# Optimization experiments

Measured on AMD Instinct MI355X. Metric: run time of the kernel, lower is better.

## Reference

```python
import jax, jax.numpy as jnp
import numpy as np

N = 32768      # points (multiple of block_size)
D = 32         # h_dim (dim_per_head, also token feature dim)
H = 8          # num_heads
C = 3          # n_hashes
BS = 128       # block_size
R = 3          # coords_dim
K = 8          # num_w_per_dist
NB = N // BS   # buckets
EPS_LN = 1e-5


def _ln(x, w, b):
    mu = x.mean(-1, keepdims=True)
    var = ((x - mu) ** 2).mean(-1, keepdims=True)
    return (x - mu) * jax.lax.rsqrt(var + EPS_LN) * w + b


def setup_inputs() -> dict:
    key = jax.random.key(0)
    ks = jax.random.split(key, 16)
    s = 0.05
    return {
        "x": jax.random.normal(ks[0], (N, D), jnp.float32),
        "coords": jax.random.uniform(ks[1], (N, R), jnp.float32),
        "combined_shifts": jax.random.randint(ks[2], (C, H, N), 0, 2048),
        "norm1_w": jnp.ones((D,), jnp.float32),
        "norm1_b": jnp.zeros((D,), jnp.float32),
        "wq": s * jax.random.normal(ks[3], (D, H * D), jnp.float32),
        "wk": s * jax.random.normal(ks[4], (D, H * D), jnp.float32),
        "wv": s * jax.random.normal(ks[5], (D, H * D), jnp.float32),
        "w_rpe_w": s * jax.random.normal(ks[6], (H * D, R * K), jnp.float32),
        "alpha": jax.random.normal(ks[7], (H, D + R, C), jnp.float32),  # E2LSH (frozen)
        "out_w": s * jax.random.normal(ks[8], (H * D, D), jnp.float32),
        "out_b": jnp.zeros((D,), jnp.float32),
        "norm2_w": jnp.ones((D,), jnp.float32),
        "norm2_b": jnp.zeros((D,), jnp.float32),
        "ff1_w": s * jax.random.normal(ks[9], (D, D), jnp.float32),
        "ff1_b": jnp.zeros((D,), jnp.float32),
        "ff2_w": s * jax.random.normal(ks[10], (D, D), jnp.float32),
        "ff2_b": jnp.zeros((D,), jnp.float32),
    }


def _to_buckets(v, perm):
    # v: [H, N, d], perm: [C, H, N] -> [C, H, NB, BS, d]
    g = jnp.take_along_axis(v[None], perm[..., None], axis=2)
    return g.reshape(C, H, NB, BS, v.shape[-1])


def _from_buckets(s, inv):
    # s: [C, H, NB, BS, d], inv: [C, H, N] -> [C, H, N, d]
    f = s.reshape(C, H, N, s.shape[-1])
    return jnp.take_along_axis(f, inv[..., None], axis=2)


def _hept_forward(x, coords, combined_shifts, norm1_w, norm1_b, wq, wk, wv,
                  w_rpe_w, alpha, out_w, out_b, norm2_w, norm2_b,
                  ff1_w, ff1_b, ff2_w, ff2_b):
    xn = _ln(x, norm1_w, norm1_b)
    q = (xn @ wq).reshape(N, H, D)
    k = (xn @ wk).reshape(N, H, D)
    v = (xn @ wv).reshape(N, H, D)

    # prep_qk: RPE-derived kernel coordinates
    w = w_rpe_w.reshape(H, D, R, K)                       # (h d) (r k) -> h d r k
    qw = jnp.exp(jnp.minimum(w.sum(axis=1), 50.0)).sum(-1)  # [H, R]
    sqrt_w_r = jnp.sqrt(2.0 * qw)[None] * coords[:, None]    # [N, H, R]
    q_hat = jnp.concatenate([q, sqrt_w_r], axis=-1)          # [N, H, D+R]
    k_hat = jnp.concatenate([k, sqrt_w_r], axis=-1)

    q_hat = jnp.transpose(q_hat, (1, 0, 2))  # [H, N, D+R]
    k_hat = jnp.transpose(k_hat, (1, 0, 2))
    val = jnp.transpose(v, (1, 0, 2))        # [H, N, D]

    # LSH hashing (no-grad in original; outputs only feed integer argsort)
    qh = jax.lax.stop_gradient(jnp.einsum('hnd,hdc->chn', q_hat, alpha))
    kh = jax.lax.stop_gradient(jnp.einsum('hnd,hdc->chn', k_hat, alpha))
    hi = jnp.maximum(qh.max(-1, keepdims=True), kh.max(-1, keepdims=True))
    lo = jnp.minimum(qh.min(-1, keepdims=True), kh.min(-1, keepdims=True))
    hash_shift = hi - lo                                    # [C, H, 1]
    shift = combined_shifts.astype(qh.dtype) * hash_shift
    q_pos = jnp.argsort(qh + shift, axis=-1)                # [C, H, N]
    k_pos = jnp.argsort(kh + shift, axis=-1)

    s_query = _to_buckets(q_hat, q_pos)
    s_key = _to_buckets(k_hat, k_pos)
    s_value = _to_buckets(val, k_pos)

    # kernelized exponential attention within buckets
    q_sq = -0.5 * (s_query ** 2).sum(-1, keepdims=True)
    k_sq = -0.5 * (s_key ** 2).sum(-1, keepdims=True)
    dists = jnp.einsum('chbid,chbjd->chbij', s_query, s_key)
    qk = jnp.exp(jnp.minimum(dists + q_sq + jnp.swapaxes(k_sq, -1, -2), 0.0))
    denom = qk.sum(-1, keepdims=True) + 1e-20
    so = jnp.einsum('chbij,chbjd->chbid', qk, s_value)

    q_rev = jnp.argsort(q_pos, axis=-1)  # inverse permutation
    o = _from_buckets(so, q_rev).sum(0)        # [H, N, D]
    logits = _from_buckets(denom, q_rev).sum(0)  # [H, N, 1]
    out = o / logits

    out = jnp.transpose(out, (1, 0, 2)).reshape(N, H * D) @ out_w + out_b
    x = x + out  # dropout is identity in eval
    xn2 = _ln(x, norm2_w, norm2_b)
    ff = jax.nn.silu(xn2 @ ff1_w + ff1_b) @ ff2_w + ff2_b
    return x + ff


def reference(x, coords, combined_shifts, norm1_w, norm1_b, wq, wk, wv,
              w_rpe_w, alpha, out_w, out_b, norm2_w, norm2_b,
              ff1_w, ff1_b, ff2_w, ff2_b):
    return _hept_forward(x, coords, combined_shifts, norm1_w, norm1_b, wq, wk, wv,
                         w_rpe_w, alpha, out_w, out_b, norm2_w, norm2_b,
                         ff1_w, ff1_b, ff2_w, ff2_b)
```

## Files before the change

kernel.cpp:

```cpp
#include <hip/hip_runtime.h>

#define NPTS 32768
#define DIM 32
#define NH 8
#define NC 3
#define BSZ 128
#define NB 256
#define DH 35
#define DP 36
#define NSEG 24

typedef unsigned long long ull;
typedef __attribute__((ext_vector_type(8))) short bf16x8;
typedef __attribute__((ext_vector_type(4))) float f32x4;

__device__ __forceinline__ unsigned fmap(float f){
  unsigned b = __float_as_uint(f);
  return (b & 0x80000000u) ? ~b : (b | 0x80000000u);
}
__device__ __forceinline__ float funmap(unsigned u){
  unsigned b = (u & 0x80000000u) ? (u & 0x7fffffffu) : ~u;
  return __uint_as_float(b);
}
__device__ __forceinline__ unsigned short f2bf(float f){
  unsigned u = __float_as_uint(f);
  u += 0x7fffu + ((u >> 16) & 1u);
  return (unsigned short)(u >> 16);
}
__device__ __forceinline__ float bf2f(unsigned short h){
  return __uint_as_float(((unsigned)h) << 16);
}
__device__ __forceinline__ void cvt8(const float* f, bf16x8& hi, bf16x8& lo){
  #pragma unroll
  for (int j = 0; j < 8; ++j){
    unsigned short hb = f2bf(f[j]);
    hi[j] = (short)hb;
    lo[j] = (short)f2bf(f[j] - bf2f(hb));
  }
}

__device__ __forceinline__ void cswap(ull& a, ull& b, bool up){
  if ((a > b) == up){ ull t = a; a = b; b = t; }
}
__device__ __forceinline__ void bitonic8_initial(ull r[8], unsigned gbase){
  #pragma unroll
  for (int p = 0; p < 4; ++p){
    bool up = (((gbase + 2*p) & 2) == 0);
    cswap(r[2*p], r[2*p+1], up);
  }
  #pragma unroll
  for (int b = 0; b < 2; ++b){
    bool up = (((gbase + 4*b) & 4) == 0);
    cswap(r[4*b+0], r[4*b+2], up);
    cswap(r[4*b+1], r[4*b+3], up);
    cswap(r[4*b+0], r[4*b+1], up);
    cswap(r[4*b+2], r[4*b+3], up);
  }
  bool up = ((gbase & 8) == 0);
  #pragma unroll
  for (int i = 0; i < 4; ++i) cswap(r[i], r[i+4], up);
  #pragma unroll
  for (int b = 0; b < 2; ++b){
    cswap(r[4*b+0], r[4*b+2], up);
    cswap(r[4*b+1], r[4*b+3], up);
  }
  #pragma unroll
  for (int p = 0; p < 4; ++p) cswap(r[2*p], r[2*p+1], up);
}
__device__ __forceinline__ void bitonic8_finish(ull r[8], bool up){
  #pragma unroll
  for (int i = 0; i < 4; ++i) cswap(r[i], r[i+4], up);
  #pragma unroll
  for (int b = 0; b < 2; ++b){
    cswap(r[4*b+0], r[4*b+2], up);
    cswap(r[4*b+1], r[4*b+3], up);
  }
  #pragma unroll
  for (int p = 0; p < 4; ++p) cswap(r[2*p], r[2*p+1], up);
}

__global__ __launch_bounds__(256) void k_prep(const float* __restrict__ w_rpe,
        float* __restrict__ qw_sqrt, unsigned* __restrict__ slots_hi,
        unsigned* __restrict__ slots_lo){
  int tid = threadIdx.x;
  if (tid < NSEG){ slots_hi[tid] = 0u; slots_lo[tid] = 0xFFFFFFFFu; }
  __shared__ float S[24][8];
  if (tid < 192){
    int hr = tid >> 3, kk = tid & 7;
    int h = hr / 3, r = hr % 3;
    float s = 0.f;
    #pragma unroll
    for (int d = 0; d < DIM; ++d) s += w_rpe[(h*DIM + d)*24 + (r*8 + kk)];
    S[hr][kk] = expf(fminf(s, 50.f));
  }
  __syncthreads();
  if (tid < 24){
    float q = 0.f;
    #pragma unroll
    for (int kk = 0; kk < 8; ++kk) q += S[tid][kk];
    qw_sqrt[tid] = sqrtf(2.f * q);
  }
}

__global__ __launch_bounds__(256) void k_qkv(const float* __restrict__ x,
        const float* __restrict__ n1w, const float* __restrict__ n1b,
        const float* __restrict__ coords, const float* __restrict__ wq,
        const float* __restrict__ wk, const float* __restrict__ wv,
        const float* __restrict__ qw_sqrt,
        float* __restrict__ q_hat, float* __restrict__ k_hat,
        float* __restrict__ val){
  __shared__ float W[3][DIM][NH*DIM];
  __shared__ float XT[128][33];
  int tid = threadIdx.x;
  for (int idx = tid; idx < 3*DIM*NH*DIM; idx += 256){
    int which = idx / (DIM*NH*DIM);
    int rem = idx % (DIM*NH*DIM);
    const float* src = which==0 ? wq : (which==1 ? wk : wv);
    W[which][rem/(NH*DIM)][rem%(NH*DIM)] = src[rem];
  }
  int base = blockIdx.x * 128;
  if (tid < 128){
    const float4* xr4 = (const float4*)(x + (size_t)(base + tid)*DIM);
    float4 v[8];
    float s = 0.f;
    #pragma unroll
    for (int u = 0; u < 8; ++u){ v[u] = xr4[u]; s += v[u].x+v[u].y+v[u].z+v[u].w; }
    float mu = s * (1.f/32.f);
    float var = 0.f;
    #pragma unroll
    for (int u = 0; u < 8; ++u){
      float a0=v[u].x-mu, a1=v[u].y-mu, a2=v[u].z-mu, a3=v[u].w-mu;
      var += a0*a0+a1*a1+a2*a2+a3*a3;
    }
    var *= (1.f/32.f);
    float rs = rsqrtf(var + 1e-5f);
    #pragma unroll
    for (int u = 0; u < 8; ++u){
      XT[tid][u*4+0] = (v[u].x-mu)*rs*n1w[u*4+0] + n1b[u*4+0];
      XT[tid][u*4+1] = (v[u].y-mu)*rs*n1w[u*4+1] + n1b[u*4+1];
      XT[tid][u*4+2] = (v[u].z-mu)*rs*n1w[u*4+2] + n1b[u*4+2];
      XT[tid][u*4+3] = (v[u].w-mu)*rs*n1w[u*4+3] + n1b[u*4+3];
    }
  }
  __syncthreads();
  int h = tid >> 5, i = tid & 31;
  #pragma unroll
  for (int rep = 0; rep < 4; ++rep){
    int tl = i + 32*rep;
    int n = base + tl;
    float xr[32];
    #pragma unroll
    for (int d = 0; d < 32; ++d) xr[d] = XT[tl][d];
    float cpart[3];
    #pragma unroll
    for (int r = 0; r < 3; ++r) cpart[r] = qw_sqrt[h*3+r] * coords[(size_t)n*3 + r];

    float* dq = q_hat + ((size_t)h*NPTS + n)*DP;
    float* dk = k_hat + ((size_t)h*NPTS + n)*DP;
    float* dv = val   + ((size_t)h*NPTS + n)*DIM;
    #pragma unroll
    for (int which = 0; which < 3; ++which){
      for (int j0 = 0; j0 < 32; j0 += 4){
        float4 acc = {0.f,0.f,0.f,0.f};
        #pragma unroll
        for (int d = 0; d < 32; ++d){
          float4 wv4 = *(const float4*)&W[which][d][h*32 + j0];
          acc.x += xr[d]*wv4.x; acc.y += xr[d]*wv4.y;
          acc.z += xr[d]*wv4.z; acc.w += xr[d]*wv4.w;
        }
        if (which == 0)      *(float4*)&dq[j0] = acc;
        else if (which == 1) *(float4*)&dk[j0] = acc;
        else                 *(float4*)&dv[j0] = acc;
      }
    }
    dq[32]=cpart[0]; dq[33]=cpart[1]; dq[34]=cpart[2]; dq[35]=0.f;
    dk[32]=cpart[0]; dk[33]=cpart[1]; dk[34]=cpart[2]; dk[35]=0.f;
  }
}

__global__ __launch_bounds__(256) void k_hash(const float* __restrict__ q_hat,
        const float* __restrict__ k_hat, const float* __restrict__ alpha,
        float* __restrict__ qh_buf, float* __restrict__ kh_buf,
        unsigned* __restrict__ slots_hi, unsigned* __restrict__ slots_lo){
  int h = blockIdx.y;
  int n = blockIdx.x*256 + threadIdx.x;
  __shared__ float A[DH][NC];
  for (int idx = threadIdx.x; idx < DH*NC; idx += 256)
    A[idx/3][idx%3] = alpha[h*DH*NC + idx];
  __syncthreads();
  float qr[36], kr[36];
  const float4* qp = (const float4*)(q_hat + ((size_t)h*NPTS + n)*DP);
  const float4* kp = (const float4*)(k_hat + ((size_t)h*NPTS + n)*DP);
  #pragma unroll
  for (int u = 0; u < 9; ++u){
    *(float4*)&qr[u*4] = qp[u];
    *(float4*)&kr[u*4] = kp[u];
  }
  #pragma unroll
  for (int c = 0; c < NC; ++c){
    float qh = 0.f, kh = 0.f;
    #pragma unroll
    for (int d = 0; d < DH; ++d){ qh += qr[d]*A[d][c]; kh += kr[d]*A[d][c]; }
    qh_buf[((size_t)(c*NH + h))*NPTS + n] = qh;
    kh_buf[((size_t)(c*NH + h))*NPTS + n] = kh;
    float hi = fmaxf(qh, kh), lo = fminf(qh, kh);
    #pragma unroll
    for (int off = 32; off; off >>= 1){
      hi = fmaxf(hi, __shfl_xor(hi, off));
      lo = fminf(lo, __shfl_xor(lo, off));
    }
    if ((threadIdx.x & 63) == 0){
      atomicMax(&slots_hi[c*NH + h], fmap(hi));
      atomicMin(&slots_lo[c*NH + h], fmap(lo));
    }
  }
}

__global__ __launch_bounds__(1024) void k_sort_pack_local(
        const float* __restrict__ qh_buf, const float* __restrict__ kh_buf,
        const int* __restrict__ shifts,
        const unsigned* __restrict__ slots_hi, const unsigned* __restrict__ slots_lo,
        ull* __restrict__ packed){
  __shared__ ull ld[9216];
  int chunk = blockIdx.x;
  int lst = chunk >> 2;
  int seg = lst < NSEG ? lst : lst - NSEG;
  const float* buf = lst < NSEG ? qh_buf : kh_buf;
  unsigned coff = (unsigned)(chunk & 3) * 8192u;
  float hs = funmap(slots_hi[seg]) - funmap(slots_lo[seg]);
  unsigned tid = threadIdx.x;

  {
    ull r[8];
    unsigned gb = coff + 8u*tid;
    #pragma unroll
    for (int e = 0; e < 8; ++e){
      unsigned n = gb + e;
      size_t gi = (size_t)seg*NPTS + n;
      float key = buf[gi] + (float)shifts[gi] * hs;
      r[e] = ((ull)fmap(key) << 32) | n;
    }
    bitonic8_initial(r, gb);
    #pragma unroll
    for (int e = 0; e < 8; ++e) ld[9u*tid + e] = r[e];
  }
  __syncthreads();

  for (unsigned k = 16; k <= 8192u; k <<= 1){
    for (unsigned j = k >> 1; j >= 8; j >>= 1){
      #pragma unroll
      for (int it = 0; it < 4; ++it){
        unsigned p = tid + 1024u*it;
        unsigned i  = ((p & ~(j-1)) << 1) | (p & (j-1));
        unsigned x2 = i | j;
        bool up = (((coff + i) & k) == 0);
        unsigned pi = i + (i>>3), px = x2 + (x2>>3);
        ull a = ld[pi], b2 = ld[px];
        if ((a > b2) == up){ ld[pi] = b2; ld[px] = a; }
      }
      __syncthreads();
    }
    {
      ull r[8];
      #pragma unroll
      for (int e = 0; e < 8; ++e) r[e] = ld[9u*tid + e];
      bool up = (((coff + 8u*tid) & k) == 0);
      bitonic8_finish(r, up);
      #pragma unroll
      for (int e = 0; e < 8; ++e) ld[9u*tid + e] = r[e];
    }
    __syncthreads();
  }
  size_t base = (size_t)lst*NPTS + coff;
  for (unsigned idx = tid; idx < 8192; idx += 1024)
    packed[base + idx] = ld[idx + (idx>>3)];
}

__global__ __launch_bounds__(1024) void k_sort_local(ull* __restrict__ data,
        unsigned k_lo, unsigned k_hi){
  __shared__ ull ld[9216];
  int chunk = blockIdx.x;
  size_t base = (size_t)chunk * 8192;
  unsigned coff = (unsigned)(chunk & 3) * 8192u;
  unsigned tid = threadIdx.x;
  for (unsigned idx = tid; idx < 8192; idx += 1024)
    ld[idx + (idx>>3)] = data[base + idx];
  __syncthreads();
  for (unsigned k = k_lo; k <= k_hi; k <<= 1){
    unsigned j0 = (k >> 1) < 4096u ? (k >> 1) : 4096u;
    for (unsigned j = j0; j >= 8; j >>= 1){
      #pragma unroll
      for (int it = 0; it < 4; ++it){
        unsigned p = tid + 1024u*it;
        unsigned i  = ((p & ~(j-1)) << 1) | (p & (j-1));
        unsigned x2 = i | j;
        bool up = (((coff + i) & k) == 0);
        unsigned pi = i + (i>>3), px = x2 + (x2>>3);
        ull a = ld[pi], b2 = ld[px];
        if ((a > b2) == up){ ld[pi] = b2; ld[px] = a; }
      }
      __syncthreads();
    }
    {
      ull r[8];
      #pragma unroll
      for (int e = 0; e < 8; ++e) r[e] = ld[9u*tid + e];
      bool up = (((coff + 8u*tid) & k) == 0);
      bitonic8_finish(r, up);
      #pragma unroll
      for (int e = 0; e < 8; ++e) ld[9u*tid + e] = r[e];
    }
    __syncthreads();
  }
  for (unsigned idx = tid; idx < 8192; idx += 1024)
    data[base + idx] = ld[idx + (idx>>3)];
}

__global__ __launch_bounds__(256) void k_sort_global(ull* __restrict__ data,
        unsigned k, unsigned j){
  unsigned t = blockIdx.x*256 + threadIdx.x;
  unsigned seg = t >> 14;
  unsigned p = t & 16383u;
  unsigned i  = ((p & ~(j-1)) << 1) | (p & (j-1));
  unsigned x2 = i | j;
  size_t base = (size_t)seg << 15;
  bool up = ((i & k) == 0);
  ull a = data[base + i], b = data[base + x2];
  if ((a > b) == up){ data[base + i] = b; data[base + x2] = a; }
}

__global__ __launch_bounds__(512, 6) void k_attn(const float* __restrict__ q_hat,
        const float* __restrict__ k_hat, const float* __restrict__ val,
        const ull* __restrict__ packed, float* __restrict__ o_acc,
        float* __restrict__ logit_acc){
  __shared__ short KP[16384];
  __shared__ short Vt[4096];

  int t = threadIdx.x;
  int blk = blockIdx.x;
  int seg = blk >> 8;
  int b = blk & 255;
  int h = seg & 7;
  const ull* pq = packed + ((size_t)seg << 15) + (size_t)b*BSZ;
  const ull* pk = packed + ((size_t)(NSEG + seg) << 15) + (size_t)b*BSZ;

  int lane = t & 63;
  int w = t >> 6;
  int l15 = lane & 15, g = lane >> 4;
  int qrow = 16*w + l15;

  unsigned iqr = (unsigned)(pq[qrow] & 0xffffffffull);
  const float* qr = q_hat + ((size_t)h*NPTS + iqr)*DP;
  float4 qa = ((const float4*)qr)[2*g];
  float4 qb = ((const float4*)qr)[2*g+1];
  float4 qt = ((const float4*)qr)[8];

  if (t < 128){
    unsigned ik = (unsigned)(pk[t] & 0xffffffffull);
    const float* kr = k_hat + ((size_t)h*NPTS + ik)*DP;
    float f[40];
    #pragma unroll
    for (int u = 0; u < 9; ++u) *(float4*)&f[u*4] = ((const float4*)kr)[u];
    float sq = 0.f;
    #pragma unroll
    for (int d = 0; d < 36; ++d) sq += f[d]*f[d];
    f[35] = -0.5f * sq;
    f[36] = 1.0f;
    f[37] = 0.f; f[38] = 0.f; f[39] = 0.f;
    int rowbase = t*64;
    int sw = (t & 7) << 3;
    #pragma unroll
    for (int c = 0; c < 40; c += 4){
      unsigned short h0=f2bf(f[c]),   h1=f2bf(f[c+1]);
      unsigned short h2=f2bf(f[c+2]), h3=f2bf(f[c+3]);
      unsigned short l0=f2bf(f[c]  -bf2f(h0)), l1=f2bf(f[c+1]-bf2f(h1));
      unsigned short l2=f2bf(f[c+2]-bf2f(h2)), l3=f2bf(f[c+3]-bf2f(h3));
      int o = rowbase + (c ^ sw);
      uint2 hv, lv;
      hv.x = (unsigned)h0 | ((unsigned)h1 << 16);
      hv.y = (unsigned)h2 | ((unsigned)h3 << 16);
      lv.x = (unsigned)l0 | ((unsigned)l1 << 16);
      lv.y = (unsigned)l2 | ((unsigned)l3 << 16);
      *(uint2*)&KP[o] = hv;
      *(uint2*)&KP[8192 + o] = lv;
    }
    #pragma unroll
    for (int c = 40; c < 64; c += 4){
      int o = rowbase + (c ^ sw);
      *(uint2*)&KP[o] = (uint2){0u,0u};
      *(uint2*)&KP[8192 + o] = (uint2){0u,0u};
    }
  } else if (t < 384){
    int r = (t - 128) & 127;
    int half = (t - 128) >> 7;
    unsigned ik = (unsigned)(pk[r] & 0xffffffffull);
    const float* vr = val + ((size_t)h*NPTS + ik)*DIM + 16*half;
    float fv[16];
    #pragma unroll
    for (int u = 0; u < 4; ++u) *(float4*)&fv[u*4] = ((const float4*)vr)[u];
    #pragma unroll
    for (int d = 0; d < 16; ++d){
      int vd = 16*half + d;
      Vt[vd*128 + (r ^ ((vd&7)<<3))] = (short)f2bf(fv[d]);
    }
  }

  float f0[8] = {qa.x,qa.y,qa.z,qa.w, qb.x,qb.y,qb.z,qb.w};
  float psq = 0.f;
  #pragma unroll
  for (int j = 0; j < 8; ++j) psq += f0[j]*f0[j];
  if (g == 0) psq += qt.x*qt.x + qt.y*qt.y + qt.z*qt.z;
  psq += __shfl_xor(psq, 16);
  psq += __shfl_xor(psq, 32);
  float qsq = -0.5f * psq;
  bf16x8 qh0, ql0, qh1, ql1;
  cvt8(f0, qh0, ql0);
  float f1[8] = {0.f,0.f,0.f,0.f,0.f,0.f,0.f,0.f};
  if (g == 0){
    f1[0] = qt.x; f1[1] = qt.y; f1[2] = qt.z;
    f1[3] = 1.0f;
    f1[4] = qsq;
  }
  cvt8(f1, qh1, ql1);

  __syncthreads();

  f32x4 acc[8];
  #pragma unroll
  for (int kt = 0; kt < 8; ++kt) acc[kt] = (f32x4){0.f,0.f,0.f,0.f};
  #pragma unroll
  for (int kt = 0; kt < 8; ++kt){
    int krow = 16*kt + l15;
    int base = krow*64;
    int sw = (krow & 7) << 3;
    bf16x8 ah0 = *(const bf16x8*)&KP[base + ((8*g) ^ sw)];
    bf16x8 ah1 = *(const bf16x8*)&KP[base + ((32 + 8*g) ^ sw)];
    bf16x8 al0 = *(const bf16x8*)&KP[8192 + base + ((8*g) ^ sw)];
    bf16x8 al1 = *(const bf16x8*)&KP[8192 + base + ((32 + 8*g) ^ sw)];
    f32x4 c = acc[kt];
    c = __builtin_amdgcn_mfma_f32_16x16x32_bf16(ah0, qh0, c, 0, 0, 0);
    c = __builtin_amdgcn_mfma_f32_16x16x32_bf16(ah1, qh1, c, 0, 0, 0);
    c = __builtin_amdgcn_mfma_f32_16x16x32_bf16(al0, qh0, c, 0, 0, 0);
    c = __builtin_amdgcn_mfma_f32_16x16x32_bf16(al1, qh1, c, 0, 0, 0);
    c = __builtin_amdgcn_mfma_f32_16x16x32_bf16(ah0, ql0, c, 0, 0, 0);
    c = __builtin_amdgcn_mfma_f32_16x16x32_bf16(ah1, ql1, c, 0, 0, 0);
    acc[kt] = c;
  }

  __syncthreads();

  int qsw = (qrow & 7) << 3;
  float dena = 0.f;
  #pragma unroll
  for (int kt = 0; kt < 8; ++kt){
    f32x4 c = acc[kt];
    float p0 = __expf(fminf(c[0], 0.f));
    float p1 = __expf(fminf(c[1], 0.f));
    float p2 = __expf(fminf(c[2], 0.f));
    float p3 = __expf(fminf(c[3], 0.f));
    dena += p0 + p1 + p2 + p3;
    int key = 16*kt + 4*g;
    uint2 pv;
    pv.x = (unsigned)f2bf(p0) | ((unsigned)f2bf(p1) << 16);
    pv.y = (unsigned)f2bf(p2) | ((unsigned)f2bf(p3) << 16);
    *(uint2*)&KP[qrow*128 + (key ^ qsw)] = pv;
  }

  f32x4 oacc[2];
  oacc[0] = (f32x4){0.f,0.f,0.f,0.f};
  oacc[1] = (f32x4){0.f,0.f,0.f,0.f};
  #pragma unroll
  for (int ks = 0; ks < 4; ++ks){
    bf16x8 pA = *(const bf16x8*)&KP[qrow*128 + ((32*ks + 8*g) ^ qsw)];
    #pragma unroll
    for (int nt = 0; nt < 2; ++nt){
      int vd = 16*nt + l15;
      bf16x8 vB = *(const bf16x8*)&Vt[vd*128 + ((32*ks + 8*g) ^ ((vd&7)<<3))];
      oacc[nt] = __builtin_amdgcn_mfma_f32_16x16x32_bf16(pA, vB, oacc[nt], 0, 0, 0);
    }
  }

  {
    float d = dena;
    d += __shfl_xor(d, 16);
    d += __shfl_xor(d, 32);
    if (lane < 16) atomicAdd(&logit_acc[(size_t)h*NPTS + iqr], d + 1e-20f);
  }
  #pragma unroll
  for (int nt = 0; nt < 2; ++nt){
    f32x4 c = oacc[nt];
    #pragma unroll
    for (int r = 0; r < 4; ++r){
      unsigned iq = (unsigned)__shfl((int)iqr, 4*g + r);
      atomicAdd(&o_acc[((size_t)h*NPTS + iq)*DIM + 16*nt + l15], c[r]);
    }
  }
}

__global__ __launch_bounds__(256) void k_final(const float* __restrict__ x,
        const float* __restrict__ o_acc, const float* __restrict__ logit_acc,
        const float* __restrict__ out_w, const float* __restrict__ out_b,
        const float* __restrict__ n2w, const float* __restrict__ n2b,
        const float* __restrict__ f1w, const float* __restrict__ f1b,
        const float* __restrict__ f2w, const float* __restrict__ f2b,
        float* __restrict__ out){
  __shared__ float OW[256][32];
  __shared__ float F1[32][32];
  __shared__ float F2[32][32];
  int tid = threadIdx.x;
  for (int idx = tid; idx < 256*32; idx += 256) OW[idx/32][idx%32] = out_w[idx];
  for (int idx = tid; idx < 1024; idx += 256){
    F1[idx/32][idx%32] = f1w[idx];
    F2[idx/32][idx%32] = f2w[idx];
  }
  __syncthreads();
  int n = blockIdx.x*256 + tid;
  float attn[32];
  #pragma unroll
  for (int j = 0; j < 32; ++j) attn[j] = out_b[j];
  for (int h = 0; h < 8; ++h){
    float inv = 1.f / logit_acc[(size_t)h*NPTS + n];
    const float4* orow = (const float4*)(o_acc + ((size_t)h*NPTS + n)*DIM);
    #pragma unroll
    for (int u = 0; u < 8; ++u){
      float4 ov = orow[u];
      float vals[4] = {ov.x*inv, ov.y*inv, ov.z*inv, ov.w*inv};
      #pragma unroll
      for (int s = 0; s < 4; ++s){
        const float* wrow = &OW[h*32 + u*4 + s][0];
        #pragma unroll
        for (int j = 0; j < 32; ++j) attn[j] += vals[s] * wrow[j];
      }
    }
  }
  const float* xp = x + (size_t)n*DIM;
  float xr[32]; float s = 0.f;
  #pragma unroll
  for (int d = 0; d < 32; ++d){ xr[d] = xp[d] + attn[d]; s += xr[d]; }
  float mu = s * (1.f/32.f);
  float var = 0.f;
  #pragma unroll
  for (int d = 0; d < 32; ++d){ float dx = xr[d]-mu; var += dx*dx; }
  var *= (1.f/32.f);
  float rs = rsqrtf(var + 1e-5f);
  float xn2[32];
  #pragma unroll
  for (int d = 0; d < 32; ++d) xn2[d] = (xr[d]-mu)*rs*n2w[d] + n2b[d];
  float z[32];
  #pragma unroll
  for (int j = 0; j < 32; ++j) z[j] = f1b[j];
  #pragma unroll
  for (int d = 0; d < 32; ++d){
    float xd = xn2[d];
    const float* wrow = &F1[d][0];
    #pragma unroll
    for (int j = 0; j < 32; ++j) z[j] += xd * wrow[j];
  }
  #pragma unroll
  for (int j = 0; j < 32; ++j) z[j] = z[j] / (1.f + __expf(-z[j]));
  float y[32];
  #pragma unroll
  for (int d = 0; d < 32; ++d) y[d] = f2b[d];
  #pragma unroll
  for (int j = 0; j < 32; ++j){
    float zj = z[j];
    const float* wrow = &F2[j][0];
    #pragma unroll
    for (int d = 0; d < 32; ++d) y[d] += zj * wrow[d];
  }
  float* op = out + (size_t)n*DIM;
  #pragma unroll
  for (int d = 0; d < 32; ++d) op[d] = xr[d] + y[d];
}

extern "C" void kernel_launch(void* const* d_in, const int* in_sizes, int n_in,
                              void* d_out, int out_size, void* d_ws, size_t ws_size,
                              hipStream_t stream){
  const float* x      = (const float*)d_in[0];
  const float* coords = (const float*)d_in[1];
  const int*   shifts = (const int*)d_in[2];
  const float* n1w    = (const float*)d_in[3];
  const float* n1b    = (const float*)d_in[4];
  const float* wq     = (const float*)d_in[5];
  const float* wk     = (const float*)d_in[6];
  const float* wv     = (const float*)d_in[7];
  const float* w_rpe  = (const float*)d_in[8];
  const float* alpha  = (const float*)d_in[9];
  const float* out_w  = (const float*)d_in[10];
  const float* out_b  = (const float*)d_in[11];
  const float* n2w    = (const float*)d_in[12];
  const float* n2b    = (const float*)d_in[13];
  const float* f1w    = (const float*)d_in[14];
  const float* f1b    = (const float*)d_in[15];
  const float* f2w    = (const float*)d_in[16];
  const float* f2b    = (const float*)d_in[17];
  float* out = (float*)d_out;

  char* ws = (char*)d_ws;
  size_t off = 0;
  auto alloc = [&](size_t bytes){ size_t o = off; off += (bytes + 255) & ~(size_t)255; return o; };
  float*    qw_sqrt   = (float*)   (ws + alloc(24*4));
  unsigned* slots_hi  = (unsigned*)(ws + alloc(24*4));
  unsigned* slots_lo  = (unsigned*)(ws + alloc(24*4));
  float*    q_hat     = (float*)   (ws + alloc((size_t)NH*NPTS*DP*4));
  float*    k_hat     = (float*)   (ws + alloc((size_t)NH*NPTS*DP*4));
  float*    val       = (float*)   (ws + alloc((size_t)NH*NPTS*DIM*4));
  float*    qh_buf    = (float*)   (ws + alloc((size_t)NSEG*NPTS*4));
  float*    kh_buf    = (float*)   (ws + alloc((size_t)NSEG*NPTS*4));
  ull*      packed    = (ull*)     (ws + alloc((size_t)2*NSEG*NPTS*8));
  float*    o_acc     = (float*)   (ws + alloc((size_t)NH*NPTS*DIM*4));
  float*    logit_acc = (float*)   (ws + alloc((size_t)NH*NPTS*4));
  if (off > ws_size) return;

  hipMemsetAsync(o_acc, 0, (size_t)NH*NPTS*DIM*4, stream);
  hipMemsetAsync(logit_acc, 0, (size_t)NH*NPTS*4, stream);

  k_prep<<<1, 256, 0, stream>>>(w_rpe, qw_sqrt, slots_hi, slots_lo);
  k_qkv<<<NPTS/128, 256, 0, stream>>>(x, n1w, n1b, coords, wq, wk, wv, qw_sqrt,
                                      q_hat, k_hat, val);
  k_hash<<<dim3(NPTS/256, NH), 256, 0, stream>>>(q_hat, k_hat, alpha, qh_buf, kh_buf,
                                                 slots_hi, slots_lo);
  k_sort_pack_local<<<2*NSEG*4, 1024, 0, stream>>>(qh_buf, kh_buf, shifts,
                                                   slots_hi, slots_lo, packed);
  k_sort_global<<<(2*NSEG*16384)/256, 256, 0, stream>>>(packed, 16384u, 8192u);
  k_sort_local<<<2*NSEG*4, 1024, 0, stream>>>(packed, 16384u, 16384u);
  k_sort_global<<<(2*NSEG*16384)/256, 256, 0, stream>>>(packed, 32768u, 16384u);
  k_sort_global<<<(2*NSEG*16384)/256, 256, 0, stream>>>(packed, 32768u, 8192u);
  k_sort_local<<<2*NSEG*4, 1024, 0, stream>>>(packed, 32768u, 32768u);

  k_attn<<<NSEG*NB, 512, 0, stream>>>(q_hat, k_hat, val, packed, o_acc, logit_acc);
  k_final<<<NPTS/256, 256, 0, stream>>>(x, o_acc, logit_acc, out_w, out_b,
                                        n2w, n2b, f1w, f1b, f2w, f2b, out);
}
```

Measured before the change: 525.7 us.

## Register-block QKV projection over four rows and spread K/V staging across all threads

The QKV projection now loads four token rows into registers and accumulates all four per weight fetch, so each LDS weight float4 is reused four times. The kernel also gets launch_bounds(256,1) to allow the extra registers. In the attention kernel, K and V bucket staging is redistributed so four threads share each key row, with the squared norm reduced by shuffles, replacing the old uneven split where a few threads did all the conversion. This aims to cut LDS traffic and staging latency, at the cost of more register pressure and possibly lower occupancy in k_qkv.

```diff
diff --git a/kernel.cpp b/kernel.cpp
--- a/kernel.cpp
+++ b/kernel.cpp
@@ -102,7 +102,7 @@
   }
 }
 
-__global__ __launch_bounds__(256) void k_qkv(const float* __restrict__ x,
+__global__ __launch_bounds__(256, 1) void k_qkv(const float* __restrict__ x,
         const float* __restrict__ n1w, const float* __restrict__ n1b,
         const float* __restrict__ coords, const float* __restrict__ wq,
         const float* __restrict__ wk, const float* __restrict__ wv,
@@ -144,37 +144,49 @@
   }
   __syncthreads();
   int h = tid >> 5, i = tid & 31;
+  float xr0[32], xr1[32], xr2[32], xr3[32];
+  #pragma unroll
+  for (int d = 0; d < 32; ++d){
+    xr0[d] = XT[i][d]; xr1[d] = XT[i+32][d];
+    xr2[d] = XT[i+64][d]; xr3[d] = XT[i+96][d];
+  }
+  float cp[4][3];
+  #pragma unroll
+  for (int rep = 0; rep < 4; ++rep)
+    #pragma unroll
+    for (int r = 0; r < 3; ++r)
+      cp[rep][r] = qw_sqrt[h*3+r] * coords[(size_t)(base + i + 32*rep)*3 + r];
+
+  #pragma unroll
+  for (int which = 0; which < 3; ++which){
+    for (int j0 = 0; j0 < 32; j0 += 4){
+      float4 a0 = {0,0,0,0}, a1 = {0,0,0,0}, a2 = {0,0,0,0}, a3 = {0,0,0,0};
+      #pragma unroll
+      for (int d = 0; d < 32; ++d){
+        float4 w4 = *(const float4*)&W[which][d][h*32 + j0];
+        a0.x += xr0[d]*w4.x; a0.y += xr0[d]*w4.y; a0.z += xr0[d]*w4.z; a0.w += xr0[d]*w4.w;
+        a1.x += xr1[d]*w4.x; a1.y += xr1[d]*w4.y; a1.z += xr1[d]*w4.z; a1.w += xr1[d]*w4.w;
+        a2.x += xr2[d]*w4.x; a2.y += xr2[d]*w4.y; a2.z += xr2[d]*w4.z; a2.w += xr2[d]*w4.w;
+        a3.x += xr3[d]*w4.x; a3.y += xr3[d]*w4.y; a3.z += xr3[d]*w4.z; a3.w += xr3[d]*w4.w;
+      }
+      #pragma unroll
+      for (int rep = 0; rep < 4; ++rep){
+        int n = base + i + 32*rep;
+        float4 a = rep==0 ? a0 : (rep==1 ? a1 : (rep==2 ? a2 : a3));
+        float* dst = which==0 ? (q_hat + ((size_t)h*NPTS + n)*DP)
+                   : (which==1 ? (k_hat + ((size_t)h*NPTS + n)*DP)
+                               : (val   + ((size_t)h*NPTS + n)*DIM));
+        *(float4*)&dst[j0] = a;
+      }
+    }
+  }
   #pragma unroll
   for (int rep = 0; rep < 4; ++rep){
-    int tl = i + 32*rep;
-    int n = base + tl;
-    float xr[32];
-    #pragma unroll
-    for (int d = 0; d < 32; ++d) xr[d] = XT[tl][d];
-    float cpart[3];
-    #pragma unroll
-    for (int r = 0; r < 3; ++r) cpart[r] = qw_sqrt[h*3+r] * coords[(size_t)n*3 + r];
-
+    int n = base + i + 32*rep;
     float* dq = q_hat + ((size_t)h*NPTS + n)*DP;
     float* dk = k_hat + ((size_t)h*NPTS + n)*DP;
-    float* dv = val   + ((size_t)h*NPTS + n)*DIM;
-    #pragma unroll
-    for (int which = 0; which < 3; ++which){
-      for (int j0 = 0; j0 < 32; j0 += 4){
-        float4 acc = {0.f,0.f,0.f,0.f};
-        #pragma unroll
-        for (int d = 0; d < 32; ++d){
-          float4 wv4 = *(const float4*)&W[which][d][h*32 + j0];
-          acc.x += xr[d]*wv4.x; acc.y += xr[d]*wv4.y;
-          acc.z += xr[d]*wv4.z; acc.w += xr[d]*wv4.w;
-        }
-        if (which == 0)      *(float4*)&dq[j0] = acc;
-        else if (which == 1) *(float4*)&dk[j0] = acc;
-        else                 *(float4*)&dv[j0] = acc;
-      }
-    }
-    dq[32]=cpart[0]; dq[33]=cpart[1]; dq[34]=cpart[2]; dq[35]=0.f;
-    dk[32]=cpart[0]; dk[33]=cpart[1]; dk[34]=cpart[2]; dk[35]=0.f;
+    dq[32]=cp[rep][0]; dq[33]=cp[rep][1]; dq[34]=cp[rep][2]; dq[35]=0.f;
+    dk[32]=cp[rep][0]; dk[33]=cp[rep][1]; dk[34]=cp[rep][2]; dk[35]=0.f;
   }
 }
 
@@ -355,26 +367,46 @@
   float4 qb = ((const float4*)qr)[2*g+1];
   float4 qt = ((const float4*)qr)[8];
 
-  if (t < 128){
-    unsigned ik = (unsigned)(pk[t] & 0xffffffffull);
+  {
+    int r = t >> 2;
+    int qd = t & 3;
+    unsigned ik = (unsigned)(pk[r] & 0xffffffffull);
     const float* kr = k_hat + ((size_t)h*NPTS + ik)*DP;
-    float f[40];
-    #pragma unroll
-    for (int u = 0; u < 9; ++u) *(float4*)&f[u*4] = ((const float4*)kr)[u];
-    float sq = 0.f;
-    #pragma unroll
-    for (int d = 0; d < 36; ++d) sq += f[d]*f[d];
-    f[35] = -0.5f * sq;
-    f[36] = 1.0f;
-    f[37] = 0.f; f[38] = 0.f; f[39] = 0.f;
-    int rowbase = t*64;
-    int sw = (t & 7) << 3;
-    #pragma unroll
-    for (int c = 0; c < 40; c += 4){
-      unsigned short h0=f2bf(f[c]),   h1=f2bf(f[c+1]);
-      unsigned short h2=f2bf(f[c+2]), h3=f2bf(f[c+3]);
-      unsigned short l0=f2bf(f[c]  -bf2f(h0)), l1=f2bf(f[c+1]-bf2f(h1));
-      unsigned short l2=f2bf(f[c+2]-bf2f(h2)), l3=f2bf(f[c+3]-bf2f(h3));
+    float fk[3] = {0.f, 0.f, 0.f};
+    float vals[16];
+    float psqk = 0.f;
+    if (qd < 2){
+      #pragma unroll
+      for (int u = 0; u < 4; ++u)
+        *(float4*)&vals[u*4] = ((const float4*)(kr + 16*qd))[u];
+      #pragma unroll
+      for (int d2 = 0; d2 < 16; ++d2) psqk += vals[d2]*vals[d2];
+    } else if (qd == 2){
+      float4 k4 = *(const float4*)(kr + 32);
+      fk[0] = k4.x; fk[1] = k4.y; fk[2] = k4.z;
+      psqk = k4.x*k4.x + k4.y*k4.y + k4.z*k4.z;
+    }
+    psqk += __shfl_xor(psqk, 1);
+    psqk += __shfl_xor(psqk, 2);
+    float ksq = -0.5f * psqk;
+    if (qd == 2){
+      vals[0]=fk[0]; vals[1]=fk[1]; vals[2]=fk[2];
+      vals[3]=ksq; vals[4]=1.0f;
+      #pragma unroll
+      for (int d2 = 5; d2 < 16; ++d2) vals[d2] = 0.f;
+    } else if (qd == 3){
+      #pragma unroll
+      for (int d2 = 0; d2 < 16; ++d2) vals[d2] = 0.f;
+    }
+    int rowbase = r*64;
+    int sw = (r & 7) << 3;
+    #pragma unroll
+    for (int c0 = 0; c0 < 16; c0 += 4){
+      int c = 16*qd + c0;
+      unsigned short h0=f2bf(vals[c0]),   h1=f2bf(vals[c0+1]);
+      unsigned short h2=f2bf(vals[c0+2]), h3=f2bf(vals[c0+3]);
+      unsigned short l0=f2bf(vals[c0]  -bf2f(h0)), l1=f2bf(vals[c0+1]-bf2f(h1));
+      unsigned short l2=f2bf(vals[c0+2]-bf2f(h2)), l3=f2bf(vals[c0+3]-bf2f(h3));
       int o = rowbase + (c ^ sw);
       uint2 hv, lv;
       hv.x = (unsigned)h0 | ((unsigned)h1 << 16);
@@ -384,24 +416,14 @@
       *(uint2*)&KP[o] = hv;
       *(uint2*)&KP[8192 + o] = lv;
     }
-    #pragma unroll
-    for (int c = 40; c < 64; c += 4){
-      int o = rowbase + (c ^ sw);
-      *(uint2*)&KP[o] = (uint2){0u,0u};
-      *(uint2*)&KP[8192 + o] = (uint2){0u,0u};
-    }
-  } else if (t < 384){
-    int r = (t - 128) & 127;
-    int half = (t - 128) >> 7;
-    unsigned ik = (unsigned)(pk[r] & 0xffffffffull);
-    const float* vr = val + ((size_t)h*NPTS + ik)*DIM + 16*half;
-    float fv[16];
-    #pragma unroll
-    for (int u = 0; u < 4; ++u) *(float4*)&fv[u*4] = ((const float4*)vr)[u];
-    #pragma unroll
-    for (int d = 0; d < 16; ++d){
-      int vd = 16*half + d;
-      Vt[vd*128 + (r ^ ((vd&7)<<3))] = (short)f2bf(fv[d]);
+    const float* vr = val + ((size_t)h*NPTS + ik)*DIM + 8*qd;
+    float fv[8];
+    *(float4*)&fv[0] = ((const float4*)vr)[0];
+    *(float4*)&fv[4] = ((const float4*)vr)[1];
+    #pragma unroll
+    for (int d2 = 0; d2 < 8; ++d2){
+      int vd = 8*qd + d2;
+      Vt[vd*128 + (r ^ ((vd&7)<<3))] = (short)f2bf(fv[d2]);
     }
   }
 
```

After: 498.9 us. 5.1% less time.
